# Performance work log

Hardware: AMD Instinct MI355X
Metric: run time of the kernel (lower is better)

## Reference

```python
import jax, jax.numpy as jnp
import numpy as np

NUM_HEADS = 12


def setup_inputs() -> dict:
    key = jax.random.key(0)
    k1, k2, k3, k4 = jax.random.split(key, 4)
    B, N, C = 32, 577, 768
    x = jax.random.normal(k1, (B, N, C), dtype=jnp.float32)
    qkv_w = jax.random.normal(k2, (3 * C, C), dtype=jnp.float32) * 0.02
    proj_w = jax.random.normal(k3, (C, C), dtype=jnp.float32) * 0.02
    proj_b = jax.random.normal(k4, (C,), dtype=jnp.float32) * 0.02
    return {"x": x, "qkv_w": qkv_w, "proj_w": proj_w, "proj_b": proj_b,
            "reduction_num": 115}


def reference(x, qkv_w, proj_w, proj_b, reduction_num):
    B, N, C = x.shape
    H = NUM_HEADS
    hd = C // H
    scale = hd ** -0.5

    # qkv projection (no bias), split into q, k, v of shape (B, H, N, hd)
    qkv = (x @ qkv_w.T).reshape(B, N, 3, H, hd)
    qkv = jnp.transpose(qkv, (2, 0, 3, 1, 4))  # (3, B, H, N, hd)
    q, k, v = qkv[0], qkv[1], qkv[2]

    attn = jax.nn.softmax(jnp.einsum('bhnd,bhmd->bhnm', q * scale, k), axis=-1)  # (B,H,N,N)

    # diagonal entries at positions 1..N-1 (skip CLS), averaged over heads
    attn_diag = jnp.diagonal(attn, axis1=-2, axis2=-1)[:, :, 1:].mean(axis=1)  # (B, N-1)

    token_rank = jnp.argsort(-attn_diag, axis=1)  # descending
    num_kept = N - reduction_num
    kept = token_rank[:, : N - 1 - reduction_num] + 1  # token indices (non-CLS)
    index_cls = jnp.zeros((B, 1), dtype=kept.dtype)
    index_kept = jnp.sort(jnp.concatenate([index_cls, kept], axis=1), axis=1)  # (B, num_kept)

    # gather kept query rows of the attention matrix: (B, H, num_kept, N)
    weight = jnp.take_along_axis(attn, index_kept[:, None, :, None], axis=2)

    out = jnp.einsum('bhkn,bhnd->bhkd', weight, v)  # (B, H, num_kept, hd)
    out = jnp.transpose(out, (0, 2, 1, 3)).reshape(B, num_kept, C)
    out = out @ proj_w.T + proj_b

    original_x = jnp.take_along_axis(x, index_kept[:, :, None], axis=1)  # (B, num_kept, C)
    return out + original_x
```

## Files before the change

kernel.cpp:

```cpp
#include <hip/hip_runtime.h>
#include <math.h>

#define BB_   32
#define NN_   577
#define CC_   768
#define HH_   12
#define HD_   64
#define NPAD  640
#define BH_   (BB_*HH_)
#define MQ    (BB_*NN_)
#define KEPT  462
#define KEPTP 464
#define MP    (BB_*KEPT)
#define TOPK  461

#define MT_   145
#define NT_   18

using short8 = __attribute__((ext_vector_type(8))) short;
using f32x4  = __attribute__((ext_vector_type(4))) float;
using u16x4  = __attribute__((ext_vector_type(4))) unsigned short;
using u32x2  = __attribute__((ext_vector_type(2))) unsigned int;

using gp1_t = const __attribute__((address_space(1))) void*;
using sp3_t = __attribute__((address_space(3))) void*;

__device__ __forceinline__ unsigned short f2bf(float f) {
  unsigned int u = __float_as_uint(f);
  u += 0x7fffu + ((u >> 16) & 1u);
  return (unsigned short)(u >> 16);
}
__device__ __forceinline__ float bf2f(unsigned short h) {
  return __uint_as_float(((unsigned int)h) << 16);
}
__device__ __forceinline__ f32x4 mfma16(short8 a, short8 b, f32x4 c) {
  return __builtin_amdgcn_mfma_f32_16x16x32_bf16(a, b, c, 0, 0, 0);
}
__device__ __forceinline__ void gl_lds16(const void* g, void* l) {
  __builtin_amdgcn_global_load_lds((gp1_t)g, (sp3_t)l, 16, 0, 0);
}

#define SC_ 0.18033688011112042f

__device__ __forceinline__ void split4(const float* __restrict__ in, int i,
                                       unsigned short* __restrict__ hi,
                                       unsigned short* __restrict__ lo) {
  f32x4 f = *(const f32x4*)(in + (size_t)i * 4);
  u16x4 hv, lv;
#pragma unroll
  for (int j = 0; j < 4; ++j) {
    unsigned short h = f2bf(f[j]);
    hv[j] = h;
    lv[j] = f2bf(f[j] - bf2f(h));
  }
  *(u16x4*)(hi + (size_t)i * 4) = hv;
  if (lo) *(u16x4*)(lo + (size_t)i * 4) = lv;
}

#define NX4_ (MQ * 768 / 4)
#define NW4_ (2304 * 768 / 4)
#define NP4_ (768 * 768 / 4)

__global__ __launch_bounds__(256) void k_split_all(
    const float* __restrict__ x, const float* __restrict__ qw,
    const float* __restrict__ pw,
    unsigned short* __restrict__ xh, unsigned short* __restrict__ xl,
    unsigned short* __restrict__ wh, unsigned short* __restrict__ wl,
    unsigned short* __restrict__ pwh) {
  int i2 = blockIdx.x * 256 + threadIdx.x;
#pragma unroll
  for (int s = 0; s < 2; ++s) {
    int i = 2 * i2 + s;
    if (i < NX4_) {
      split4(x, i, xh, xl);
    } else if (i < NX4_ + NW4_) {
      split4(qw, i - NX4_, wh, wl);
    } else if (i < NX4_ + NW4_ + NP4_) {
      split4(pw, i - NX4_ - NW4_, pwh, (unsigned short*)nullptr);
    }
  }
}

__global__ __launch_bounds__(256, 2) void k_qkv(
    const unsigned short* __restrict__ xh, const unsigned short* __restrict__ xl,
    const unsigned short* __restrict__ wh, const unsigned short* __restrict__ wl,
    unsigned short* __restrict__ qh, unsigned short* __restrict__ ql,
    unsigned short* __restrict__ kh, unsigned short* __restrict__ kl,
    unsigned short* __restrict__ vt) {
  __shared__ char smem[65536];
  unsigned short* lAh = (unsigned short*)smem;
  unsigned short* lAl = (unsigned short*)(smem + 16384);
  unsigned short* lBh = (unsigned short*)(smem + 32768);
  unsigned short* lBl = (unsigned short*)(smem + 49152);

  const int tid = threadIdx.x;
  const int wave = tid >> 6, lane = tid & 63, lr = lane & 15, lg = lane >> 4;
  const int wm = wave >> 1, wn = wave & 1;

  const int nwg = MT_ * NT_;
  const int qq = nwg >> 3, rr = nwg & 7;
  int orig = blockIdx.x;
  int xcd = orig & 7, pos = orig >> 3;
  int wgid = (xcd < rr ? xcd * (qq + 1) : rr * (qq + 1) + (xcd - rr) * qq) + pos;
  const int mt = wgid / NT_, nt = wgid - mt * NT_;
  const int m0 = mt * 128, n0 = nt * 128;
  const int which = n0 / 768;
  const bool three = (which < 2);

  f32x4 zf = {0.f, 0.f, 0.f, 0.f};
  f32x4 acc[4][4];
#pragma unroll
  for (int a = 0; a < 4; ++a)
#pragma unroll
    for (int bq = 0; bq < 4; ++bq) acc[a][bq] = zf;

  for (int ks = 0; ks < 12; ++ks) {
    const int k0 = ks * 64;
#pragma unroll
    for (int it = 0; it < 4; ++it) {
      int c = it * 256 + tid;
      int row = c >> 3, slot = c & 7;
      int grow = m0 + row; if (grow > MQ - 1) grow = MQ - 1;
      int gk = k0 + ((slot ^ (row & 7)) << 3);
      gl_lds16(xh + (size_t)grow * 768 + gk,
               (char*)lAh + (it * 256 + wave * 64) * 16);
      if (three)
        gl_lds16(xl + (size_t)grow * 768 + gk,
                 (char*)lAl + (it * 256 + wave * 64) * 16);
    }
#pragma unroll
    for (int it = 0; it < 4; ++it) {
      int c = it * 256 + tid;
      int row = c >> 3, slot = c & 7;
      int gn = n0 + row;
      int gk = k0 + ((slot ^ (row & 7)) << 3);
      gl_lds16(wh + (size_t)gn * 768 + gk,
               (char*)lBh + (it * 256 + wave * 64) * 16);
      if (three)
        gl_lds16(wl + (size_t)gn * 768 + gk,
                 (char*)lBl + (it * 256 + wave * 64) * 16);
    }
    __syncthreads();

#pragma unroll
    for (int kk = 0; kk < 2; ++kk) {
      short8 fa[4], fal[4], fb[4], fbl[4];
#pragma unroll
      for (int ms = 0; ms < 4; ++ms) {
        int row = wm * 64 + ms * 16 + lr;
        int off = (kk * 64 + lg * 16) ^ ((row & 7) << 4);
        fa[ms] = *(const short8*)((const char*)lAh + row * 128 + off);
        if (three) fal[ms] = *(const short8*)((const char*)lAl + row * 128 + off);
      }
#pragma unroll
      for (int ns = 0; ns < 4; ++ns) {
        int row = wn * 64 + ns * 16 + lr;
        int off = (kk * 64 + lg * 16) ^ ((row & 7) << 4);
        fb[ns] = *(const short8*)((const char*)lBh + row * 128 + off);
        if (three) fbl[ns] = *(const short8*)((const char*)lBl + row * 128 + off);
      }
#pragma unroll
      for (int ms = 0; ms < 4; ++ms)
#pragma unroll
        for (int ns = 0; ns < 4; ++ns) {
          acc[ms][ns] = mfma16(fa[ms], fb[ns], acc[ms][ns]);
          if (three) {
            acc[ms][ns] = mfma16(fa[ms], fbl[ns], acc[ms][ns]);
            acc[ms][ns] = mfma16(fal[ms], fb[ns], acc[ms][ns]);
          }
        }
    }
    __syncthreads();
  }

  if (which < 2) {
    float* lC = (float*)smem;
    for (int p = 0; p < 2; ++p) {
      if (p) __syncthreads();
      if (wn == p) {
#pragma unroll
        for (int ms = 0; ms < 4; ++ms)
#pragma unroll
          for (int ns = 0; ns < 4; ++ns) {
            int r = wm * 64 + ms * 16 + 4 * lg;
            int cc = ns * 16 + lr;
#pragma unroll
            for (int reg = 0; reg < 4; ++reg)
              lC[(r + reg) * 66 + cc] = acc[ms][ns][reg];
          }
      }
      __syncthreads();
      const int h = ((n0 % 768) >> 6) + p;
      int r = tid >> 1, c0 = (tid & 1) * 32;
      int m = m0 + r;
      if (m < MQ) {
        int b = m / 577, n = m % 577;
        size_t base = ((size_t)(b * 12 + h) * NPAD + n) * 64 + c0;
        unsigned short* dh = (which == 0 ? qh : kh) + base;
        unsigned short* dl = (which == 0 ? ql : kl) + base;
#pragma unroll
        for (int cc = 0; cc < 32; cc += 4) {
          u16x4 hv, lv;
#pragma unroll
          for (int j = 0; j < 4; ++j) {
            float f = lC[r * 66 + c0 + cc + j];
            unsigned short hh = f2bf(f);
            hv[j] = hh;
            lv[j] = f2bf(f - bf2f(hh));
          }
          *(u16x4*)(dh + cc) = hv;
          *(u16x4*)(dl + cc) = lv;
        }
      }
    }
  } else {
    const int h0 = (n0 % 768) >> 6;
#pragma unroll
    for (int ms = 0; ms < 4; ++ms)
#pragma unroll
      for (int ns = 0; ns < 4; ++ns) {
        int m = m0 + wm * 64 + ms * 16 + 4 * lg;
        int c = wn * 64 + ns * 16 + lr;
        int h = h0 + (c >> 6), d = c & 63;
        int b = m / 577, n = m - b * 577;
        if (m + 3 < MQ && n + 3 < 577) {
          u16x4 pv;
#pragma unroll
          for (int reg = 0; reg < 4; ++reg) pv[reg] = f2bf(acc[ms][ns][reg]);
          *(u16x4*)(vt + ((size_t)(b * 12 + h) * 64 + d) * NPAD + n) = pv;
        } else {
#pragma unroll
          for (int reg = 0; reg < 4; ++reg) {
            int mm = m + reg;
            if (mm < MQ) {
              int bb = mm / 577, nn = mm - bb * 577;
              vt[((size_t)(bb * 12 + h) * 64 + d) * NPAD + nn] = f2bf(acc[ms][ns][reg]);
            }
          }
        }
      }
  }
}

__global__ __launch_bounds__(256) void k_attn1(
    const unsigned short* __restrict__ qh, const unsigned short* __restrict__ ql,
    const unsigned short* __restrict__ kh, const unsigned short* __restrict__ kl,
    const unsigned short* __restrict__ vt, float* __restrict__ S0,
    float* __restrict__ Dg, unsigned short* __restrict__ Ob) {
  __shared__ char smem[45056];
  char* lK = smem;
  char* lV = smem + 16384;
  char* lP = smem + 24576;

  int wgid = (blockIdx.x & 7) * 240 + (blockIdx.x >> 3);
  const int bh = wgid / 5;
  const int i0 = (wgid - bh * 5) * 128;
  const int tid = threadIdx.x, w = tid >> 6, lane = tid & 63;
  const int lr = lane & 15, lg = lane >> 4;
  const size_t qb = (size_t)bh * NPAD * 64;

  bool act[2];
#pragma unroll
  for (int iu = 0; iu < 2; ++iu) act[iu] = (i0 + w * 32 + iu * 16) < NN_;

  const int krow = tid >> 3, kslot = tid & 7;
  const int vrow = tid >> 2, vslot = tid & 3;
  const size_t ksrc = (size_t)krow * 64 + ((kslot ^ (krow & 7)) << 3);
  const size_t vsrc = ((size_t)bh * 64 + vrow) * NPAD + ((vslot ^ (vrow & 3)) << 3);

  short8 qf[2][2], qfl[2][2];
#pragma unroll
  for (int iu = 0; iu < 2; ++iu) {
    const size_t qrow = qb + (size_t)(i0 + w * 32 + iu * 16 + lr) * 64;
#pragma unroll
    for (int kk = 0; kk < 2; ++kk) {
      qf[iu][kk]  = *(const short8*)(qh + qrow + kk * 32 + lg * 8);
      qfl[iu][kk] = *(const short8*)(ql + qrow + kk * 32 + lg * 8);
    }
  }
  f32x4 zf = {0.f, 0.f, 0.f, 0.f};
  f32x4 oacc[2][4];
#pragma unroll
  for (int iu = 0; iu < 2; ++iu)
#pragma unroll
    for (int ds = 0; ds < 4; ++ds) oacc[iu][ds] = zf;
  float s0[2] = {0.0f, 0.0f};

  gl_lds16(kh + qb + ksrc, lK + tid * 16);
  gl_lds16(kl + qb + ksrc, lK + 4096 + tid * 16);
  gl_lds16(vt + vsrc, lV + tid * 16);
  __syncthreads();

  int buf = 0, pb = 0;
  char* lPw = lP + w * 5120;
  for (int jp = 0; jp < 19; ++jp) {
    if (jp < 18) {
      int jn = (jp + 1) * 32;
      gl_lds16(kh + qb + (size_t)jn * 64 + ksrc, lK + (buf ^ 1) * 8192 + tid * 16);
      gl_lds16(kl + qb + (size_t)jn * 64 + ksrc, lK + (buf ^ 1) * 8192 + 4096 + tid * 16);
      gl_lds16(vt + vsrc + jn, lV + (buf ^ 1) * 4096 + tid * 16);
    }
#pragma unroll
    for (int t = 0; t < 2; ++t) {
      const int jloc = t * 16 + lr;
      short8 kfh[2], kfl2[2];
#pragma unroll
      for (int kk = 0; kk < 2; ++kk) {
        int off = (kk * 64 + lg * 16) ^ ((jloc & 7) << 4);
        kfh[kk]  = *(const short8*)(lK + buf * 8192 + jloc * 128 + off);
        kfl2[kk] = *(const short8*)(lK + buf * 8192 + 4096 + jloc * 128 + off);
      }
      int jbase = jp * 32 + t * 16 + 4 * lg;
#pragma unroll
      for (int iu = 0; iu < 2; ++iu) {
        if (act[iu]) {
          f32x4 c = zf;
          __builtin_amdgcn_s_setprio(1);
#pragma unroll
          for (int kk = 0; kk < 2; ++kk) {
            c = mfma16(kfh[kk], qfl[iu][kk], c);
            c = mfma16(kfl2[kk], qf[iu][kk], c);
            c = mfma16(kfh[kk], qf[iu][kk], c);
          }
          __builtin_amdgcn_s_setprio(0);
          float p0 = (jbase + 0 < 577) ? exp2f(c[0] * SC_) : 0.0f;
          float p1 = (jbase + 1 < 577) ? exp2f(c[1] * SC_) : 0.0f;
          float p2 = (jbase + 2 < 577) ? exp2f(c[2] * SC_) : 0.0f;
          float p3 = (jbase + 3 < 577) ? exp2f(c[3] * SC_) : 0.0f;
          s0[iu] += (p0 + p1) + (p2 + p3);
          u32x2 wv;
          wv[0] = (unsigned)f2bf(p0) | ((unsigned)f2bf(p1) << 16);
          wv[1] = (unsigned)f2bf(p2) | ((unsigned)f2bf(p3) << 16);
          *(u32x2*)(lPw + iu * 2560 + pb * 1280 + lr * 80 + t * 32 + lg * 8) = wv;
        }
      }
    }
    asm volatile("" ::: "memory");
#pragma unroll
    for (int iu = 0; iu < 2; ++iu) {
      if (act[iu]) {
        short8 pa = *(const short8*)(lPw + iu * 2560 + pb * 1280 + lr * 80 + lg * 16);
        __builtin_amdgcn_s_setprio(1);
#pragma unroll
        for (int ds = 0; ds < 4; ++ds) {
          int r = ds * 16 + lr;
          int off = (lg * 16) ^ ((r & 3) << 4);
          short8 vf = *(const short8*)(lV + buf * 4096 + r * 64 + off);
          oacc[iu][ds] = mfma16(pa, vf, oacc[iu][ds]);
        }
        __builtin_amdgcn_s_setprio(0);
      }
    }
    asm volatile("" ::: "memory");
    pb ^= 1;
    __syncthreads();
    buf ^= 1;
  }

#pragma unroll
  for (int iu = 0; iu < 2; ++iu) {
    if (!act[iu]) continue;
    float s = s0[iu];
    s += __shfl_xor(s, 16);
    s += __shfl_xor(s, 32);
    const int iw = i0 + w * 32 + iu * 16;
    if (lg == 0) S0[(size_t)bh * NPAD + iw + lr] = s;
    float rs[4];
#pragma unroll
    for (int reg = 0; reg < 4; ++reg) rs[reg] = 1.0f / __shfl(s, 4 * lg + reg);
#pragma unroll
    for (int ds = 0; ds < 4; ++ds)
#pragma unroll
      for (int reg = 0; reg < 4; ++reg)
        Ob[((size_t)bh * NPAD + iw + 4 * lg + reg) * 64 + ds * 16 + lr] =
            f2bf(oacc[iu][ds][reg] * rs[reg]);
  }

#pragma unroll
  for (int rr = 0; rr < 2; ++rr) {
    const int row = i0 + rr * 64 + (tid >> 2);
    const int c = tid & 3;
    const size_t base = qb + (size_t)row * 64 + c * 16;
    short8 a0 = *(const short8*)(qh + base), a1 = *(const short8*)(qh + base + 8);
    short8 b0 = *(const short8*)(ql + base), b1 = *(const short8*)(ql + base + 8);
    short8 c0 = *(const short8*)(kh + base), c1 = *(const short8*)(kh + base + 8);
    short8 d0 = *(const short8*)(kl + base), d1 = *(const short8*)(kl + base + 8);
    float acc = 0.0f;
#pragma unroll
    for (int j = 0; j < 8; ++j) {
      float qv = bf2f((unsigned short)a0[j]) + bf2f((unsigned short)b0[j]);
      float kv = bf2f((unsigned short)c0[j]) + bf2f((unsigned short)d0[j]);
      acc += qv * kv;
      float qv1 = bf2f((unsigned short)a1[j]) + bf2f((unsigned short)b1[j]);
      float kv1 = bf2f((unsigned short)c1[j]) + bf2f((unsigned short)d1[j]);
      acc += qv1 * kv1;
    }
    acc += __shfl_xor(acc, 1, 4);
    acc += __shfl_xor(acc, 2, 4);
    if (c == 0) Dg[(size_t)bh * NPAD + row] = acc * SC_;
  }
}

__global__ __launch_bounds__(576) void k_select(const float* __restrict__ Dg,
                                                const float* __restrict__ S0,
                                                int* __restrict__ idxk) {
  __shared__ float kbuf[576];
  __shared__ int kflag[576];
  int b = blockIdx.x, t = threadIdx.x;
  if (t < 576) {
    float a = 0.0f;
#pragma unroll
    for (int h = 0; h < 12; ++h) {
      size_t o = (size_t)(b * 12 + h) * NPAD + t + 1;
      a += exp2f(Dg[o]) / S0[o];
    }
    kbuf[t] = a;
  }
  __syncthreads();
  if (t < 576) {
    float kt = kbuf[t];
    int cnt = 0;
    for (int j = 0; j < 576; ++j) {
      float kj = kbuf[j];
      cnt += (kj > kt || (kj == kt && j < t)) ? 1 : 0;
    }
    kflag[t] = (cnt < TOPK) ? 1 : 0;
  }
  __syncthreads();
  if (t < 576 && kflag[t]) {
    int pos = 1;
    for (int j = 0; j < t; ++j) pos += kflag[j];
    idxk[b * KEPTP + pos] = t + 1;
  }
  if (t == 0) {
    idxk[b * KEPTP + 0] = 0;
    idxk[b * KEPTP + 462] = 0;
    idxk[b * KEPTP + 463] = 0;
  }
}

__global__ __launch_bounds__(256) void k_proj(
    const unsigned short* __restrict__ Ob, const unsigned short* __restrict__ pwh,
    const float* __restrict__ pb, const float* __restrict__ x,
    const int* __restrict__ idxk, float* __restrict__ out) {
  __shared__ char smem[33792];
  unsigned short* lA = (unsigned short*)smem;
  unsigned short* lB = (unsigned short*)(smem + 16384);
  const int tid = threadIdx.x;
  const int wave = tid >> 6, lane = tid & 63, lr = lane & 15, lg = lane >> 4;
  const int wm = wave >> 1, wn = wave & 1;
  int wgid = (blockIdx.x & 7) * 87 + (blockIdx.x >> 3);
  const int mt = wgid / 6, nt = wgid - mt * 6;
  const int m0 = mt * 128, n0 = nt * 128;

  int tokr[4], bbr[4], offr8[4];
#pragma unroll
  for (int it = 0; it < 4; ++it) {
    int c = it * 256 + tid;
    int row = c >> 3, slot = c & 7;
    int m = m0 + row; if (m > MP - 1) m = MP - 1;
    int bb = m / 462, tt = m - bb * 462;
    tokr[it] = idxk[bb * KEPTP + tt];
    bbr[it] = bb;
    offr8[it] = (slot ^ (row & 7)) << 3;
  }

  f32x4 zf = {0.f, 0.f, 0.f, 0.f};
  f32x4 acc[4][4];
#pragma unroll
  for (int a = 0; a < 4; ++a)
#pragma unroll
    for (int bq = 0; bq < 4; ++bq) acc[a][bq] = zf;

  for (int ks = 0; ks < 12; ++ks) {
    int k0 = ks * 64;
#pragma unroll
    for (int it = 0; it < 4; ++it) {
      gl_lds16(Ob + ((size_t)(bbr[it] * 12 + ks) * NPAD + tokr[it]) * 64 + offr8[it],
               (char*)lA + (it * 256 + wave * 64) * 16);
    }
#pragma unroll
    for (int it = 0; it < 4; ++it) {
      int c = it * 256 + tid;
      int row = c >> 3, slot = c & 7;
      int gk = k0 + ((slot ^ (row & 7)) << 3);
      gl_lds16(pwh + (size_t)(n0 + row) * 768 + gk,
               (char*)lB + (it * 256 + wave * 64) * 16);
    }
    __syncthreads();
#pragma unroll
    for (int kk = 0; kk < 2; ++kk) {
      short8 fa[4], fb[4];
#pragma unroll
      for (int ms = 0; ms < 4; ++ms) {
        int row = wm * 64 + ms * 16 + lr;
        int off = (kk * 64 + lg * 16) ^ ((row & 7) << 4);
        fa[ms] = *(const short8*)((const char*)lA + row * 128 + off);
      }
#pragma unroll
      for (int ns = 0; ns < 4; ++ns) {
        int row = wn * 64 + ns * 16 + lr;
        int off = (kk * 64 + lg * 16) ^ ((row & 7) << 4);
        fb[ns] = *(const short8*)((const char*)lB + row * 128 + off);
      }
#pragma unroll
      for (int ms = 0; ms < 4; ++ms)
#pragma unroll
        for (int ns = 0; ns < 4; ++ns)
          acc[ms][ns] = mfma16(fa[ms], fb[ns], acc[ms][ns]);
    }
    __syncthreads();
  }

  float* lC = (float*)smem;
  for (int p = 0; p < 2; ++p) {
    if (p) __syncthreads();
    if (wn == p) {
#pragma unroll
      for (int ms = 0; ms < 4; ++ms)
#pragma unroll
        for (int ns = 0; ns < 4; ++ns) {
          int r = wm * 64 + ms * 16 + 4 * lg;
          int cc = ns * 16 + lr;
#pragma unroll
          for (int reg = 0; reg < 4; ++reg)
            lC[(r + reg) * 66 + cc] = acc[ms][ns][reg];
        }
    }
    __syncthreads();
    int r = tid >> 1, c0 = (tid & 1) * 32;
    int m = m0 + r;
    if (m < MP) {
      int bb = m / 462, tt = m % 462;
      int tok = idxk[bb * KEPTP + tt];
      int col = n0 + p * 64 + c0;
      const float* xs = x + ((size_t)(bb * 577) + tok) * 768 + col;
      float* dst = out + (size_t)m * 768 + col;
#pragma unroll
      for (int cc = 0; cc < 32; cc += 4) {
        f32x4 xv = *(const f32x4*)(xs + cc);
        f32x4 bv = *(const f32x4*)(pb + col + cc);
        f32x4 o;
#pragma unroll
        for (int j = 0; j < 4; ++j)
          o[j] = lC[r * 66 + c0 + cc + j] + bv[j] + xv[j];
        *(f32x4*)(dst + cc) = o;
      }
    }
  }
}

extern "C" void kernel_launch(void* const* d_in, const int* in_sizes, int n_in,
                              void* d_out, int out_size, void* d_ws, size_t ws_size,
                              hipStream_t stream) {
  const float* x  = (const float*)d_in[0];
  const float* qw = (const float*)d_in[1];
  const float* pw = (const float*)d_in[2];
  const float* pb = (const float*)d_in[3];
  (void)in_sizes; (void)n_in; (void)out_size; (void)ws_size;

  char* ws = (char*)d_ws;
  size_t off = 0;
  auto alloc = [&](size_t bytes) {
    void* p = ws + off;
    off += (bytes + 255) & ~(size_t)255;
    return p;
  };
  unsigned short* xh  = (unsigned short*)alloc((size_t)MQ * 768 * 2);
  unsigned short* xl  = (unsigned short*)alloc((size_t)MQ * 768 * 2);
  unsigned short* wh  = (unsigned short*)alloc((size_t)2304 * 768 * 2);
  unsigned short* wl  = (unsigned short*)alloc((size_t)2304 * 768 * 2);
  unsigned short* pwh = (unsigned short*)alloc((size_t)768 * 768 * 2);
  unsigned short* qhp = (unsigned short*)alloc((size_t)BH_ * NPAD * 64 * 2);
  unsigned short* qlp = (unsigned short*)alloc((size_t)BH_ * NPAD * 64 * 2);
  unsigned short* khp = (unsigned short*)alloc((size_t)BH_ * NPAD * 64 * 2);
  unsigned short* klp = (unsigned short*)alloc((size_t)BH_ * NPAD * 64 * 2);
  unsigned short* vtp = (unsigned short*)alloc((size_t)BH_ * NPAD * 64 * 2);
  unsigned short* Obf = (unsigned short*)alloc((size_t)BH_ * NPAD * 64 * 2);
  float* S0  = (float*)alloc((size_t)BH_ * NPAD * 4);
  float* Dg  = (float*)alloc((size_t)BH_ * NPAD * 4);
  int*   idxk = (int*)alloc((size_t)BB_ * KEPTP * 4);

  k_split_all<<<dim3(((NX4_ + NW4_ + NP4_) / 2 + 255) / 256), 256, 0, stream>>>(
      x, qw, pw, xh, xl, wh, wl, pwh);
  k_qkv<<<dim3(MT_ * NT_), 256, 0, stream>>>(xh, xl, wh, wl, qhp, qlp, khp, klp, vtp);
  k_attn1<<<dim3(1920), 256, 0, stream>>>(qhp, qlp, khp, klp, vtp, S0, Dg, Obf);
  k_select<<<dim3(32), 576, 0, stream>>>(Dg, S0, idxk);
  k_proj<<<dim3(696), 256, 0, stream>>>(Obf, pwh, pb, x, idxk, (float*)d_out);
}
```

Before: 384.7 us.

## Triple-buffer K/V tiles in attention kernel with partial vmcnt waits

```diff
diff --git a/kernel.cpp b/kernel.cpp
--- a/kernel.cpp
+++ b/kernel.cpp
@@ -247,10 +247,10 @@
     const unsigned short* __restrict__ kh, const unsigned short* __restrict__ kl,
     const unsigned short* __restrict__ vt, float* __restrict__ S0,
     float* __restrict__ Dg, unsigned short* __restrict__ Ob) {
-  __shared__ char smem[45056];
+  __shared__ char smem[47104];
   char* lK = smem;
-  char* lV = smem + 16384;
-  char* lP = smem + 24576;
+  char* lV = smem + 24576;
+  char* lP = smem + 36864;
 
   int wgid = (blockIdx.x & 7) * 240 + (blockIdx.x >> 3);
   const int bh = wgid / 5;
@@ -289,17 +289,22 @@
   gl_lds16(kh + qb + ksrc, lK + tid * 16);
   gl_lds16(kl + qb + ksrc, lK + 4096 + tid * 16);
   gl_lds16(vt + vsrc, lV + tid * 16);
-  __syncthreads();
-
-  int buf = 0, pb = 0;
-  char* lPw = lP + w * 5120;
+  gl_lds16(kh + qb + (size_t)32 * 64 + ksrc, lK + 8192 + tid * 16);
+  gl_lds16(kl + qb + (size_t)32 * 64 + ksrc, lK + 8192 + 4096 + tid * 16);
+  gl_lds16(vt + vsrc + 32, lV + 4096 + tid * 16);
+  asm volatile("s_waitcnt vmcnt(3)\n\ts_barrier" ::: "memory");
+
+  int bc = 0, bs = 2;
+  char* lPw = lP + w * 2560;
   for (int jp = 0; jp < 19; ++jp) {
-    if (jp < 18) {
-      int jn = (jp + 1) * 32;
-      gl_lds16(kh + qb + (size_t)jn * 64 + ksrc, lK + (buf ^ 1) * 8192 + tid * 16);
-      gl_lds16(kl + qb + (size_t)jn * 64 + ksrc, lK + (buf ^ 1) * 8192 + 4096 + tid * 16);
-      gl_lds16(vt + vsrc + jn, lV + (buf ^ 1) * 4096 + tid * 16);
-    }
+    if (jp <= 16) {
+      int jn = (jp + 2) * 32;
+      gl_lds16(kh + qb + (size_t)jn * 64 + ksrc, lK + bs * 8192 + tid * 16);
+      gl_lds16(kl + qb + (size_t)jn * 64 + ksrc, lK + bs * 8192 + 4096 + tid * 16);
+      gl_lds16(vt + vsrc + jn, lV + bs * 4096 + tid * 16);
+    }
+    const char* bK = lK + bc * 8192;
+    const char* bV = lV + bc * 4096;
 #pragma unroll
     for (int t = 0; t < 2; ++t) {
       const int jloc = t * 16 + lr;
@@ -307,22 +312,20 @@
 #pragma unroll
       for (int kk = 0; kk < 2; ++kk) {
         int off = (kk * 64 + lg * 16) ^ ((jloc & 7) << 4);
-        kfh[kk]  = *(const short8*)(lK + buf * 8192 + jloc * 128 + off);
-        kfl2[kk] = *(const short8*)(lK + buf * 8192 + 4096 + jloc * 128 + off);
+        kfh[kk]  = *(const short8*)(bK + jloc * 128 + off);
+        kfl2[kk] = *(const short8*)(bK + 4096 + jloc * 128 + off);
       }
       int jbase = jp * 32 + t * 16 + 4 * lg;
 #pragma unroll
       for (int iu = 0; iu < 2; ++iu) {
         if (act[iu]) {
           f32x4 c = zf;
-          __builtin_amdgcn_s_setprio(1);
 #pragma unroll
           for (int kk = 0; kk < 2; ++kk) {
             c = mfma16(kfh[kk], qfl[iu][kk], c);
             c = mfma16(kfl2[kk], qf[iu][kk], c);
             c = mfma16(kfh[kk], qf[iu][kk], c);
           }
-          __builtin_amdgcn_s_setprio(0);
           float p0 = (jbase + 0 < 577) ? exp2f(c[0] * SC_) : 0.0f;
           float p1 = (jbase + 1 < 577) ? exp2f(c[1] * SC_) : 0.0f;
           float p2 = (jbase + 2 < 577) ? exp2f(c[2] * SC_) : 0.0f;
@@ -331,7 +334,7 @@
           u32x2 wv;
           wv[0] = (unsigned)f2bf(p0) | ((unsigned)f2bf(p1) << 16);
           wv[1] = (unsigned)f2bf(p2) | ((unsigned)f2bf(p3) << 16);
-          *(u32x2*)(lPw + iu * 2560 + pb * 1280 + lr * 80 + t * 32 + lg * 8) = wv;
+          *(u32x2*)(lPw + iu * 1280 + lr * 80 + t * 32 + lg * 8) = wv;
         }
       }
     }
@@ -339,22 +342,23 @@
 #pragma unroll
     for (int iu = 0; iu < 2; ++iu) {
       if (act[iu]) {
-        short8 pa = *(const short8*)(lPw + iu * 2560 + pb * 1280 + lr * 80 + lg * 16);
-        __builtin_amdgcn_s_setprio(1);
+        short8 pa = *(const short8*)(lPw + iu * 1280 + lr * 80 + lg * 16);
 #pragma unroll
         for (int ds = 0; ds < 4; ++ds) {
           int r = ds * 16 + lr;
           int off = (lg * 16) ^ ((r & 3) << 4);
-          short8 vf = *(const short8*)(lV + buf * 4096 + r * 64 + off);
+          short8 vf = *(const short8*)(bV + r * 64 + off);
           oacc[iu][ds] = mfma16(pa, vf, oacc[iu][ds]);
         }
-        __builtin_amdgcn_s_setprio(0);
-      }
-    }
-    asm volatile("" ::: "memory");
-    pb ^= 1;
-    __syncthreads();
-    buf ^= 1;
+      }
+    }
+    if (jp <= 16) {
+      asm volatile("s_waitcnt vmcnt(3)\n\ts_barrier" ::: "memory");
+    } else if (jp == 17) {
+      asm volatile("s_waitcnt vmcnt(0)\n\ts_barrier" ::: "memory");
+    }
+    bc = (bc == 2) ? 0 : bc + 1;
+    bs = (bs == 2) ? 0 : bs + 1;
   }
 
 #pragma unroll
```

New measurement: 388.1 us. No clear change (+0.9%).
